# Kernel optimization log

Hardware: AMD Instinct MI355X
Metric: run time of the kernel (lower is better)

## Reference

```python
import jax, jax.numpy as jnp
import numpy as np

B, T, H = 128, 64, 128  # batch == decoder_num_hidden == encoder_num_hidden (forced by the module's math)


def setup_inputs() -> dict:
    key = jax.random.key(0)
    ks = jax.random.split(key, 14)
    f = lambda k, s: jax.random.normal(k, s, dtype=jnp.float32)
    W_SCALE = 0.05  # keep tanh/sigmoid/softmax away from saturation
    return {
        "X_encoded": f(ks[0], (B, T, H)),
        "X_tilde": f(ks[1], (B, T, H)),
        "W1": f(ks[2], (H, 3 * H)) * W_SCALE,   # attn_layer Linear(2*dec+enc -> enc)
        "b1": f(ks[3], (H,)) * W_SCALE,
        "W2": f(ks[4], (1, H)) * W_SCALE,        # attn_layer Linear(enc -> 1)
        "b2": f(ks[5], (1,)) * W_SCALE,
        "Wfc": f(ks[6], (1, 2 * H)) * W_SCALE,   # fc Linear(2*dec -> 1)
        "bfc": f(ks[7], (1,)) * W_SCALE,
        "Wih": f(ks[8], (4 * H, 1)) * W_SCALE,   # LSTM weight_ih, input_size=1
        "bih": f(ks[9], (4 * H,)) * W_SCALE,
        "Whh": f(ks[10], (4 * H, H)) * W_SCALE,  # LSTM weight_hh
        "bhh": f(ks[11], (4 * H,)) * W_SCALE,
        "Wfin": f(ks[12], (1, 2 * H)) * W_SCALE, # fc_final Linear(dec+enc -> 1)
        "bfin": f(ks[13], (1,)) * W_SCALE,
    }


def reference(X_encoded, X_tilde, W1, b1, W2, b2, Wfc, bfc, Wih, bih, Whh, bhh, Wfin, bfin):
    Bv, Tv, E = X_encoded.shape
    Hd = Whh.shape[1]

    def step(carry, xt):
        h, cc, _ = carry  # h: hidden d_n [B,Hd], cc: cell c_n [B,Hd]
        # x = cat(d_n broadcast over T, c_n broadcast over T, X_encoded) -> [B,T,2Hd+E]
        x = jnp.concatenate([
            jnp.broadcast_to(h[:, None, :], (Bv, Tv, Hd)),
            jnp.broadcast_to(cc[:, None, :], (Bv, Tv, Hd)),
            X_encoded], axis=2)
        a = jnp.tanh(x @ W1.T + b1) @ W2.T + b2      # [B,T,1]
        beta = jax.nn.softmax(a[..., 0], axis=1)       # [B,T]
        context = jnp.einsum('bt,bte->be', beta, X_encoded)  # [B,E]
        # cat along dim 0 then transpose: feature axis of fc is the doubled batch axis
        y = jnp.concatenate([context, xt], axis=0).T @ Wfc.T + bfc  # [E,1]
        # LSTM cell (PyTorch gate order i,f,g,o); LSTM batch == E == B
        gates = y @ Wih.T + bih + h @ Whh.T + bhh     # [E,4Hd]
        i, fg, g, o = jnp.split(gates, 4, axis=1)
        cc2 = jax.nn.sigmoid(fg) * cc + jax.nn.sigmoid(i) * jnp.tanh(g)
        h2 = jax.nn.sigmoid(o) * jnp.tanh(cc2)
        return (h2, cc2, context), None

    init = (jnp.zeros((Bv, Hd), X_encoded.dtype),
            jnp.zeros((Bv, Hd), X_encoded.dtype),
            jnp.zeros((Bv, E), X_encoded.dtype))
    (h, cc, context), _ = jax.lax.scan(step, init, jnp.swapaxes(X_tilde, 0, 1))
    return jnp.concatenate([h, context], axis=1) @ Wfin.T + bfin  # [B,1]
```

## Files before the change

### kernel.cpp

```cpp
#include <hip/hip_runtime.h>

#define TT   64
#define HD   128
#define BB   128
#define NBLK 128
#define NT   512

typedef unsigned int u32;
typedef _Float16 half2v __attribute__((ext_vector_type(2)));

#if defined(__has_builtin)
#  if __has_builtin(__builtin_amdgcn_fdot2)
#    define FDOT2(a,b,c) __builtin_amdgcn_fdot2((a),(b),(c),false)
#  endif
#endif
#ifndef FDOT2
#  define FDOT2(a,b,c) ((c) + (float)(a).x*(float)(b).x + (float)(a).y*(float)(b).y)
#endif

__device__ __forceinline__ float fast_rcp(float x){ return __builtin_amdgcn_rcpf(x); }
__device__ __forceinline__ float fast_tanh(float x){
    float e = __expf(2.f*x);
    return 1.f - 2.f*__builtin_amdgcn_rcpf(e+1.f);
}
__device__ __forceinline__ float fast_sigmoid(float x){
    return __builtin_amdgcn_rcpf(1.f + __expf(-x));
}
__device__ __forceinline__ u32 packh2(float a, float b){
    half2v v; v.x = (_Float16)a; v.y = (_Float16)b;
    return __builtin_bit_cast(u32, v);
}


__global__ void k_prep(unsigned int* __restrict__ cnt){
    if (threadIdx.x < TT) cnt[threadIdx.x] = 0u;
}

__global__ __launch_bounds__(256) void k_pre(const float* __restrict__ Xe,
    const float* __restrict__ W1, const float* __restrict__ b1,
    float* __restrict__ preE){
    __shared__ float2 sx2[16*HD];
    __shared__ float  red[512];
    const int tid = threadIdx.x;
    const int k = tid & 127, q = tid >> 7;
    const int r0 = blockIdx.x * 32;
    float wv[64];
    { const float4* wp = (const float4*)(W1 + (size_t)k*384 + 256 + q*64);
      #pragma unroll
      for (int c=0;c<16;c++){ float4 v=wp[c]; wv[4*c]=v.x; wv[4*c+1]=v.y; wv[4*c+2]=v.z; wv[4*c+3]=v.w; } }
    const float b1k = b1[k];
    float* sxf = (float*)sx2;
    for (int i=tid; i<32*HD; i+=256){
        int row = i>>7, m = i&127;
        sxf[((row>>1)*HD + m)*2 + (row&1)] = Xe[(size_t)(r0+row)*HD + m];
    }
    __syncthreads();
    for (int p=0;p<16;p++){
        const float2* xp = sx2 + p*HD + q*64;
        float a0=0.f, a1=0.f;
        #pragma unroll
        for (int i=0;i<64;i++){ float2 xv = xp[i]; a0 += xv.x*wv[i]; a1 += xv.y*wv[i]; }
        red[tid] = a0; red[256+tid] = a1;
        __syncthreads();
        if (tid<128){
            float s0 = red[tid]     + red[128+tid];
            float s1 = red[256+tid] + red[384+tid];
            preE[(size_t)(r0+2*p  )*HD + tid] = s0 + b1k;
            preE[(size_t)(r0+2*p+1)*HD + tid] = s1 + b1k;
        }
        __syncthreads();
    }
}

__global__ __launch_bounds__(128) void k_y(const float* __restrict__ Xt,
    const float* __restrict__ Wfc, const float* __restrict__ bfc,
    float* __restrict__ y){
    const int t = blockIdx.x, e = threadIdx.x;
    float acc = bfc[0];
    #pragma unroll 8
    for (int b=0;b<BB;b++)
        acc += Xt[((size_t)b*TT + t)*HD + e] * Wfc[BB+b];
    y[t*HD + e] = acc;
}

__global__ __launch_bounds__(NT,2) void k_loop(
    const float* __restrict__ Xe, const float* __restrict__ preE,
    const float* __restrict__ W1, const float* __restrict__ Whh,
    const float* __restrict__ W2, const float* __restrict__ b2,
    const float* __restrict__ Wfc,
    const float* __restrict__ Wih, const float* __restrict__ bih,
    const float* __restrict__ bhh,
    const float* __restrict__ Wfin, const float* __restrict__ bfin,
    float* __restrict__ y, unsigned int* __restrict__ cnt,
    float* __restrict__ out)
{
    extern __shared__ u32 dyn[];
    u32* sWhh2 = dyn;
    u32* spre2 = dyn + 64*512;
    __shared__ float sh[HD], scc[HD];
    __shared__ u32 shp[64], sccp[64];
    __shared__ float shW1[HD];
    __shared__ float sa[TT], sbeta[TT], sctx[HD];
    __shared__ float red[NT];
    __shared__ float sWih[NT], sbihh[NT], sW2[HD], sWfin[2*HD];
    __shared__ float sy1[1];

    const int tid = threadIdx.x;
    const int g   = blockIdx.x;
    const int k = tid & 127, mq = tid >> 7;

    {
        const float2* wr = (const float2*)(Whh + (size_t)tid*HD);
        #pragma unroll 8
        for (int kk=0;kk<64;kk++){
            float2 v = wr[kk];
            sWhh2[kk*NT + tid] = packh2(v.x, v.y);
        }
    }
    {
        const float4* pr = (const float4*)(preE + (size_t)g*TT*HD + tid*16);
        float4 a=pr[0], b=pr[1], c=pr[2], d=pr[3];
        uint4* dst = (uint4*)(spre2 + tid*8);
        dst[0] = make_uint4(packh2(a.x,a.y), packh2(a.z,a.w), packh2(b.x,b.y), packh2(b.z,b.w));
        dst[1] = make_uint4(packh2(c.x,c.y), packh2(c.z,c.w), packh2(d.x,d.y), packh2(d.z,d.w));
    }
    u32 w1r[32];
    {
        const float4* wp = (const float4*)(W1 + (size_t)k*384 + mq*64);
        #pragma unroll
        for (int c=0;c<16;c++){
            float4 v = wp[c];
            w1r[2*c]   = packh2(v.x, v.y);
            w1r[2*c+1] = packh2(v.z, v.w);
        }
    }
    sWih[tid]  = Wih[tid];
    sbihh[tid] = bih[tid] + bhh[tid];
    if (tid < HD){ sW2[tid]=W2[tid]; sh[tid]=0.f; scc[tid]=0.f; }
    if (tid < 64){ shp[tid]=0u; sccp[tid]=0u; }
    if (tid < 2*HD) sWfin[tid]=Wfin[tid];
    const float b2v  = b2[0];
    const float wfcg = Wfc[g];
    __syncthreads();

    for (int t=0;t<TT;t++){
        {
            const u32* xp = (mq<2) ? (shp + (mq&1)*32) : (sccp + (mq&1)*32);
            float acc=0.f;
            #pragma unroll
            for (int i=0;i<32;i++){
                half2v w = __builtin_bit_cast(half2v, w1r[i]);
                half2v x = __builtin_bit_cast(half2v, xp[i]);
                acc = FDOT2(w, x, acc);
            }
            red[tid]=acc;
        }
        __syncthreads();
        if (tid<HD) shW1[tid] = red[tid]+red[HD+tid]+red[2*HD+tid]+red[3*HD+tid];
        __syncthreads();

        {
            const int tp = tid>>3, kp = tid&7;
            const u32* pp = spre2 + tp*64 + kp*8;
            uint4 r0 = ((const uint4*)pp)[0];
            uint4 r1 = ((const uint4*)pp)[1];
            const int kb = kp*16;
            float acc=0.f;
            #define TERM(u,j) { half2v hv=__builtin_bit_cast(half2v,(u)); \
                acc += sW2[kb+(j)  ]*fast_tanh((float)hv.x + shW1[kb+(j)  ]); \
                acc += sW2[kb+(j)+1]*fast_tanh((float)hv.y + shW1[kb+(j)+1]); }
            TERM(r0.x,0)  TERM(r0.y,2)  TERM(r0.z,4)   TERM(r0.w,6)
            TERM(r1.x,8)  TERM(r1.y,10) TERM(r1.z,12)  TERM(r1.w,14)
            #undef TERM
            acc += __shfl_xor(acc,1); acc += __shfl_xor(acc,2); acc += __shfl_xor(acc,4);
            if (kp==0) sa[tp] = acc + b2v;
        }
        __syncthreads();

        if (tid<TT){
            float v = sa[tid];
            float mx=v;
            #pragma unroll
            for (int d=32;d;d>>=1) mx=fmaxf(mx,__shfl_xor(mx,d));
            float e=__expf(v-mx);
            float s=e;
            #pragma unroll
            for (int d=32;d;d>>=1) s+=__shfl_xor(s,d);
            sbeta[tid]=e*fast_rcp(s);
        }
        __syncthreads();

        {
            const int e=tid&127, tq=tid>>7;
            const float* xr = Xe + ((size_t)g*TT + tq*16)*HD + e;
            float acc=0.f;
            #pragma unroll
            for (int c=0;c<16;c++) acc += sbeta[tq*16+c]*xr[c*HD];
            red[tid]=acc;
        }
        __syncthreads();
        if (tid<HD){
            float cv = red[tid]+red[HD+tid]+red[2*HD+tid]+red[3*HD+tid];
            sctx[tid]=cv;
            unsafeAtomicAdd(&y[t*HD + tid], cv*wfcg);
        }

        float gj=0.f;
        {
            #pragma unroll 16
            for (int kk=0;kk<64;kk++){
                half2v w = __builtin_bit_cast(half2v, sWhh2[kk*NT + tid]);
                half2v h = __builtin_bit_cast(half2v, shp[kk]);
                gj = FDOT2(w, h, gj);
            }
        }
        asm volatile("s_waitcnt vmcnt(0)" ::: "memory");
        __syncthreads();
        if (tid==0){
            __hip_atomic_fetch_add(&cnt[t], 1u, __ATOMIC_RELAXED, __HIP_MEMORY_SCOPE_AGENT);
            while (__hip_atomic_load(&cnt[t], __ATOMIC_RELAXED, __HIP_MEMORY_SCOPE_AGENT) != (unsigned)NBLK)
                __builtin_amdgcn_s_sleep(1);
            sy1[0] = __hip_atomic_load(&y[t*HD + g], __ATOMIC_RELAXED, __HIP_MEMORY_SCOPE_AGENT);
        }
        __syncthreads();

        red[tid] = gj + sy1[0]*sWih[tid] + sbihh[tid];
        __syncthreads();
        if (tid<HD){
            float gi=red[tid], gf=red[HD+tid], gg=red[2*HD+tid], go=red[3*HD+tid];
            float c2 = fast_sigmoid(gf)*scc[tid] + fast_sigmoid(gi)*fast_tanh(gg);
            float h2 = fast_sigmoid(go)*fast_tanh(c2);
            sh[tid]=h2; scc[tid]=c2;
            float hodd = __shfl_xor(h2,1);
            float codd = __shfl_xor(c2,1);
            if (!(tid&1)){
                shp[tid>>1]  = packh2(h2, hodd);
                sccp[tid>>1] = packh2(c2, codd);
            }
        }
        __syncthreads();
    }

    if (tid<HD){
        float p = sh[tid]*sWfin[tid] + sctx[tid]*sWfin[HD+tid];
        #pragma unroll
        for (int d=32;d;d>>=1) p += __shfl_xor(p,d);
        if ((tid&63)==0) red[tid>>6]=p;
    }
    __syncthreads();
    if (tid==0) out[g] = red[0]+red[1]+bfin[0];
}

extern "C" void kernel_launch(void* const* d_in, const int* in_sizes, int n_in,
                              void* d_out, int out_size, void* d_ws, size_t ws_size,
                              hipStream_t stream){
    const float* Xe  = (const float*)d_in[0];
    const float* Xt  = (const float*)d_in[1];
    const float* W1  = (const float*)d_in[2];
    const float* b1  = (const float*)d_in[3];
    const float* W2  = (const float*)d_in[4];
    const float* b2  = (const float*)d_in[5];
    const float* Wfc = (const float*)d_in[6];
    const float* bfc = (const float*)d_in[7];
    const float* Wih = (const float*)d_in[8];
    const float* bih = (const float*)d_in[9];
    const float* Whh = (const float*)d_in[10];
    const float* bhh = (const float*)d_in[11];
    const float* Wfin= (const float*)d_in[12];
    const float* bfin= (const float*)d_in[13];

    float* ws   = (float*)d_ws;
    float* preE = ws;
    float* y    = preE + (size_t)BB*TT*HD;
    unsigned int* cnt = (unsigned int*)(y + TT*HD);
    float* outp = (float*)d_out;

    const size_t dynLds = (size_t)(64*NT + 64*64)*sizeof(u32);
    (void)hipFuncSetAttribute((const void*)k_loop,
        hipFuncAttributeMaxDynamicSharedMemorySize, (int)dynLds);

    hipLaunchKernelGGL(k_prep, dim3(1),    dim3(64),  0, stream, cnt);
    hipLaunchKernelGGL(k_pre,  dim3(256),  dim3(256), 0, stream, Xe, W1, b1, preE);
    hipLaunchKernelGGL(k_y,    dim3(TT),   dim3(128), 0, stream, Xt, Wfc, bfc, y);
    hipLaunchKernelGGL(k_loop, dim3(NBLK), dim3(NT),  dynLds, stream,
        Xe, preE, W1, Whh, W2, b2, Wfc, Wih, bih, bhh, Wfin, bfin,
        y, cnt, outp);
}
```

Measured before the change: 672.5 us.

## Replace counter barrier and atomic-add reduction with tagged per-block mailbox exchange

The per-timestep grid barrier (an atomic counter that one thread spins on) and the float atomicAdd into y are replaced by a double-buffered mailbox. Each block stores a 64-bit word holding the step tag and its partial value into a slot for each destination block. Each destination block then polls its own row with 64 lanes until every tag matches, and reduces the values with shuffles. This removes the k_prep launch and the serialized atomic traffic, and makes the reduction order deterministic. The cost is more global stores per step and a wider polling read. The Whh LDS layout is also widened to uint2 so the recurrent dot product issues half as many shared-memory loads.

```diff
diff --git a/kernel.cpp b/kernel.cpp
--- a/kernel.cpp
+++ b/kernel.cpp
@@ -7,6 +7,7 @@
 #define NT   512
 
 typedef unsigned int u32;
+typedef unsigned long long u64;
 typedef _Float16 half2v __attribute__((ext_vector_type(2)));
 
 #if defined(__has_builtin)
@@ -30,11 +31,8 @@
     half2v v; v.x = (_Float16)a; v.y = (_Float16)b;
     return __builtin_bit_cast(u32, v);
 }
-
-
-__global__ void k_prep(unsigned int* __restrict__ cnt){
-    if (threadIdx.x < TT) cnt[threadIdx.x] = 0u;
-}
+__device__ __forceinline__ half2v ash2(u32 u){ return __builtin_bit_cast(half2v, u); }
+
 
 __global__ __launch_bounds__(256) void k_pre(const float* __restrict__ Xe,
     const float* __restrict__ W1, const float* __restrict__ b1,
@@ -72,15 +70,15 @@
     }
 }
 
-__global__ __launch_bounds__(128) void k_y(const float* __restrict__ Xt,
+__global__ __launch_bounds__(128) void k_xtw(const float* __restrict__ Xt,
     const float* __restrict__ Wfc, const float* __restrict__ bfc,
-    float* __restrict__ y){
+    float* __restrict__ xtwT){
     const int t = blockIdx.x, e = threadIdx.x;
     float acc = bfc[0];
     #pragma unroll 8
     for (int b=0;b<BB;b++)
         acc += Xt[((size_t)b*TT + t)*HD + e] * Wfc[BB+b];
-    y[t*HD + e] = acc;
+    xtwT[(size_t)e*TT + t] = acc;
 }
 
 __global__ __launch_bounds__(NT,2) void k_loop(
@@ -91,18 +89,18 @@
     const float* __restrict__ Wih, const float* __restrict__ bih,
     const float* __restrict__ bhh,
     const float* __restrict__ Wfin, const float* __restrict__ bfin,
-    float* __restrict__ y, unsigned int* __restrict__ cnt,
-    float* __restrict__ out)
+    const float* __restrict__ xtwT,
+    u64* __restrict__ Ptv, float* __restrict__ out)
 {
     extern __shared__ u32 dyn[];
-    u32* sWhh2 = dyn;
-    u32* spre2 = dyn + 64*512;
+    uint2* sWhh4 = (uint2*)dyn;
+    u32*   spre2 = dyn + 2*32*NT;
     __shared__ float sh[HD], scc[HD];
     __shared__ u32 shp[64], sccp[64];
     __shared__ float shW1[HD];
     __shared__ float sa[TT], sbeta[TT], sctx[HD];
     __shared__ float red[NT];
-    __shared__ float sWih[NT], sbihh[NT], sW2[HD], sWfin[2*HD];
+    __shared__ float sWih[NT], sbihh[NT], sW2[HD], sWfin[2*HD], sxtw[TT];
     __shared__ float sy1[1];
 
     const int tid = threadIdx.x;
@@ -110,11 +108,11 @@
     const int k = tid & 127, mq = tid >> 7;
 
     {
-        const float2* wr = (const float2*)(Whh + (size_t)tid*HD);
+        const float4* wr = (const float4*)(Whh + (size_t)tid*HD);
         #pragma unroll 8
-        for (int kk=0;kk<64;kk++){
-            float2 v = wr[kk];
-            sWhh2[kk*NT + tid] = packh2(v.x, v.y);
+        for (int c=0;c<32;c++){
+            float4 v = wr[c];
+            sWhh4[c*NT + tid] = make_uint2(packh2(v.x,v.y), packh2(v.z,v.w));
         }
     }
     {
@@ -137,22 +135,21 @@
     sWih[tid]  = Wih[tid];
     sbihh[tid] = bih[tid] + bhh[tid];
     if (tid < HD){ sW2[tid]=W2[tid]; sh[tid]=0.f; scc[tid]=0.f; }
-    if (tid < 64){ shp[tid]=0u; sccp[tid]=0u; }
+    if (tid < 64){ shp[tid]=0u; sccp[tid]=0u; sxtw[tid]=xtwT[(size_t)g*TT + tid]; }
     if (tid < 2*HD) sWfin[tid]=Wfin[tid];
     const float b2v  = b2[0];
     const float wfcg = Wfc[g];
     __syncthreads();
 
     for (int t=0;t<TT;t++){
+        u64* Pcur = Ptv + (size_t)(t&1)*BB*BB;
+
         {
             const u32* xp = (mq<2) ? (shp + (mq&1)*32) : (sccp + (mq&1)*32);
             float acc=0.f;
             #pragma unroll
-            for (int i=0;i<32;i++){
-                half2v w = __builtin_bit_cast(half2v, w1r[i]);
-                half2v x = __builtin_bit_cast(half2v, xp[i]);
-                acc = FDOT2(w, x, acc);
-            }
+            for (int i=0;i<32;i++)
+                acc = FDOT2(ash2(w1r[i]), ash2(xp[i]), acc);
             red[tid]=acc;
         }
         __syncthreads();
@@ -166,7 +163,7 @@
             uint4 r1 = ((const uint4*)pp)[1];
             const int kb = kp*16;
             float acc=0.f;
-            #define TERM(u,j) { half2v hv=__builtin_bit_cast(half2v,(u)); \
+            #define TERM(u,j) { half2v hv=ash2(u); \
                 acc += sW2[kb+(j)  ]*fast_tanh((float)hv.x + shW1[kb+(j)  ]); \
                 acc += sW2[kb+(j)+1]*fast_tanh((float)hv.y + shW1[kb+(j)+1]); }
             TERM(r0.x,0)  TERM(r0.y,2)  TERM(r0.z,4)   TERM(r0.w,6)
@@ -202,25 +199,35 @@
         if (tid<HD){
             float cv = red[tid]+red[HD+tid]+red[2*HD+tid]+red[3*HD+tid];
             sctx[tid]=cv;
-            unsafeAtomicAdd(&y[t*HD + tid], cv*wfcg);
+            u64 pk = ((u64)(u32)(t+1)<<32) | (u64)__float_as_uint(cv*wfcg);
+            __hip_atomic_store(&Pcur[(size_t)tid*BB + g], pk,
+                               __ATOMIC_RELAXED, __HIP_MEMORY_SCOPE_AGENT);
         }
 
         float gj=0.f;
         {
-            #pragma unroll 16
-            for (int kk=0;kk<64;kk++){
-                half2v w = __builtin_bit_cast(half2v, sWhh2[kk*NT + tid]);
-                half2v h = __builtin_bit_cast(half2v, shp[kk]);
-                gj = FDOT2(w, h, gj);
+            #pragma unroll 8
+            for (int c=0;c<32;c++){
+                uint2 wv = sWhh4[c*NT + tid];
+                gj = FDOT2(ash2(wv.x), ash2(shp[2*c  ]), gj);
+                gj = FDOT2(ash2(wv.y), ash2(shp[2*c+1]), gj);
             }
         }
-        asm volatile("s_waitcnt vmcnt(0)" ::: "memory");
-        __syncthreads();
-        if (tid==0){
-            __hip_atomic_fetch_add(&cnt[t], 1u, __ATOMIC_RELAXED, __HIP_MEMORY_SCOPE_AGENT);
-            while (__hip_atomic_load(&cnt[t], __ATOMIC_RELAXED, __HIP_MEMORY_SCOPE_AGENT) != (unsigned)NBLK)
-                __builtin_amdgcn_s_sleep(1);
-            sy1[0] = __hip_atomic_load(&y[t*HD + g], __ATOMIC_RELAXED, __HIP_MEMORY_SCOPE_AGENT);
+
+        if (tid<64){
+            const u64* row = Pcur + (size_t)g*BB;
+            const u32 tag = (u32)(t+1);
+            u64 a,b;
+            for(;;){
+                a = __hip_atomic_load(&row[2*tid  ], __ATOMIC_RELAXED, __HIP_MEMORY_SCOPE_AGENT);
+                b = __hip_atomic_load(&row[2*tid+1], __ATOMIC_RELAXED, __HIP_MEMORY_SCOPE_AGENT);
+                bool ok = ((u32)(a>>32)==tag) & ((u32)(b>>32)==tag);
+                if (__all(ok)) break;
+            }
+            float v = __uint_as_float((u32)a) + __uint_as_float((u32)b);
+            #pragma unroll
+            for (int d=32;d;d>>=1) v += __shfl_xor(v,d);
+            if (tid==0) sy1[0] = v + sxtw[t];
         }
         __syncthreads();
 
@@ -271,18 +278,17 @@
 
     float* ws   = (float*)d_ws;
     float* preE = ws;
-    float* y    = preE + (size_t)BB*TT*HD;
-    unsigned int* cnt = (unsigned int*)(y + TT*HD);
+    u64*  Ptv   = (u64*)(preE + (size_t)BB*TT*HD);
+    float* xtwT = (float*)(Ptv + (size_t)2*BB*BB);
     float* outp = (float*)d_out;
 
     const size_t dynLds = (size_t)(64*NT + 64*64)*sizeof(u32);
     (void)hipFuncSetAttribute((const void*)k_loop,
         hipFuncAttributeMaxDynamicSharedMemorySize, (int)dynLds);
 
-    hipLaunchKernelGGL(k_prep, dim3(1),    dim3(64),  0, stream, cnt);
     hipLaunchKernelGGL(k_pre,  dim3(256),  dim3(256), 0, stream, Xe, W1, b1, preE);
-    hipLaunchKernelGGL(k_y,    dim3(TT),   dim3(128), 0, stream, Xt, Wfc, bfc, y);
+    hipLaunchKernelGGL(k_xtw,  dim3(TT),   dim3(128), 0, stream, Xt, Wfc, bfc, xtwT);
     hipLaunchKernelGGL(k_loop, dim3(NBLK), dim3(NT),  dynLds, stream,
         Xe, preE, W1, Whh, W2, b2, Wfc, Wih, bih, bhh, Wfin, bfin,
-        y, cnt, outp);
-}
+        xtwT, Ptv, outp);
+}
```

Measured after the change: 743.3 us. 10.5% more time.
